# Kernel tuning notes

Hardware: AMD Instinct MI355X
Metric: run time of the kernel (lower is better)

Reference implementation:

```python
import jax, jax.numpy as jnp
import numpy as np

N = 50000
E = 800000
D_IN = 128
D_HID = 128
N_CLASSES = 40


def setup_inputs() -> dict:
    key = jax.random.key(0)
    ks = jax.random.split(key, 8)
    features = jax.random.normal(ks[0], (N, D_IN), dtype=jnp.float32)
    src = jax.random.randint(ks[1], (E,), 0, N)
    dst = jax.random.randint(ks[2], (E,), 0, N)
    edge_index = jnp.stack([src, dst]).astype(jnp.int64)
    def glorot(k, fan_in, fan_out):
        return jax.random.normal(k, (fan_in, fan_out), dtype=jnp.float32) * (1.0 / np.sqrt(fan_in))
    W1 = glorot(ks[3], D_IN, D_HID)
    W2 = glorot(ks[4], D_HID, D_HID)
    W3 = glorot(ks[5], D_HID, N_CLASSES)
    return {
        "features": features,
        "edge_index": edge_index,
        "W1": W1, "b1": jnp.zeros((D_HID,), jnp.float32),
        "W2": W2, "b2": jnp.zeros((D_HID,), jnp.float32),
        "W3": W3, "b3": jnp.zeros((N_CLASSES,), jnp.float32),
    }


def reference(features, edge_index, W1, b1, W2, b2, W3, b3):
    # DGL GraphConv with norm='both': h = D_out^{-1/2} A^T D_in^{-1/2} ... i.e.
    # out[v] = deg_in(v)^{-1/2} * sum_{(u->v) in E} deg_out(u)^{-1/2} * x[u], then @ W + b
    src, dst = edge_index[0], edge_index[1]
    n = features.shape[0]
    ones = jnp.ones((src.shape[0],), features.dtype)
    deg_out = jnp.maximum(jax.ops.segment_sum(ones, src, num_segments=n), 1.0)
    deg_in = jnp.maximum(jax.ops.segment_sum(ones, dst, num_segments=n), 1.0)
    norm_src = deg_out ** -0.5  # [N]
    norm_dst = deg_in ** -0.5   # [N]

    def conv(x, W, b):
        msg = (x * norm_src[:, None])[src]                      # [E, d] gather
        agg = jax.ops.segment_sum(msg, dst, num_segments=n)     # [N, d] scatter-add
        return (agg * norm_dst[:, None]) @ W + b

    # bns=False default -> BatchNorm skipped; dropout p=0.0 -> identity
    h = jax.nn.relu(conv(features, W1, b1))
    h = jax.nn.relu(conv(h, W2, b2))
    return conv(h, W3, b3)  # [N, n_classes]
```

## Files before the change

kernel.cpp:

```cpp
#include <hip/hip_runtime.h>


#define EPB 4096
#define SCAN_CHUNK 4096

typedef short v8s __attribute__((ext_vector_type(8)));
typedef float v4f __attribute__((ext_vector_type(4)));

__device__ __forceinline__ ushort f2bf(float f) {
    unsigned u = __float_as_uint(f);
    unsigned r = (u + 0x7fffu + ((u >> 16) & 1u)) >> 16;
    return (ushort)r;
}
__device__ __forceinline__ void unpack2(unsigned w, float& lo, float& hi) {
    lo = __uint_as_float(w << 16);
    hi = __uint_as_float(w & 0xffff0000u);
}

__global__ __launch_bounds__(256) void front_kernel(const int* __restrict__ ei, int E,
        int nblk1, int NB, int* __restrict__ hist_all,
        ushort* __restrict__ rankD, ushort* __restrict__ rankS,
        const float* __restrict__ W1, const float* __restrict__ W2,
        const float* __restrict__ W3,
        ushort* __restrict__ W1f, ushort* __restrict__ W2f, ushort* __restrict__ W3f) {
    __shared__ int hd[512];
    __shared__ int hs[512];
    int t = threadIdx.x;
    if ((int)blockIdx.x >= nblk1) {
        int idx = ((int)blockIdx.x - nblk1) * 256 + t;
        const float* W; ushort* Wf; int Dout, NF, base;
        if (idx < 2048)      { W = W1; Wf = W1f; Dout = 128; NF = 8; base = idx; }
        else if (idx < 4096) { W = W2; Wf = W2f; Dout = 128; NF = 8; base = idx - 2048; }
        else if (idx < 5120) { W = W3; Wf = W3f; Dout = 40;  NF = 4; base = idx - 4096; }
        else return;
        int lane = base & 63;
        int f = (base >> 6) % NF;
        int ks = base / (64 * NF);
        int c = f * 16 + (lane & 15);
        int kbase = ks * 32 + (lane >> 4) * 8;
        unsigned p[4];
        #pragma unroll
        for (int j = 0; j < 4; ++j) {
            float wlo = (c < Dout) ? W[(size_t)(kbase + 2 * j) * Dout + c] : 0.f;
            float whi = (c < Dout) ? W[(size_t)(kbase + 2 * j + 1) * Dout + c] : 0.f;
            p[j] = (unsigned)f2bf(wlo) | ((unsigned)f2bf(whi) << 16);
        }
        *reinterpret_cast<uint4*>(Wf + (size_t)base * 8) = make_uint4(p[0], p[1], p[2], p[3]);
        return;
    }
    int blk = blockIdx.x;
    for (int i = t; i < 512; i += 256) { hd[i] = 0; hs[i] = 0; }
    __syncthreads();
    int base = blk * EPB;
    #pragma unroll
    for (int j = 0; j < 16; ++j) {
        int e = base + j * 256 + t;
        if (e < E) {
            int s = ei[e], d = ei[E + e];
            rankS[e] = (ushort)atomicAdd(&hs[s >> 8], 1);
            rankD[e] = (ushort)atomicAdd(&hd[d >> 8], 1);
        }
    }
    __syncthreads();
    int L = NB * nblk1;
    for (int b = t; b < NB; b += 256) {
        hist_all[b * nblk1 + blk]     = hd[b];
        hist_all[L + b * nblk1 + blk] = hs[b];
    }
}

__global__ __launch_bounds__(256) void scanA_kernel(const int* __restrict__ data, int L2,
                                                    int* __restrict__ partials) {
    __shared__ int red[256];
    int t = threadIdx.x;
    int base = blockIdx.x * SCAN_CHUNK;
    int s = 0;
    for (int i = t; i < SCAN_CHUNK; i += 256) {
        int idx = base + i;
        if (idx < L2) s += data[idx];
    }
    red[t] = s;
    __syncthreads();
    for (int off = 128; off > 0; off >>= 1) {
        if (t < off) red[t] += red[t + off];
        __syncthreads();
    }
    if (t == 0) partials[blockIdx.x] = red[0];
}

__global__ __launch_bounds__(256) void scanB_kernel(int* __restrict__ partials, int nparts) {
    __shared__ int s[256];
    int t = threadIdx.x;
    s[t] = (t < nparts) ? partials[t] : 0;
    __syncthreads();
    for (int off = 1; off < 256; off <<= 1) {
        int v = (t >= off) ? s[t - off] : 0;
        __syncthreads();
        s[t] += v;
        __syncthreads();
    }
    if (t < nparts) partials[t] = s[t] - partials[t];
}

__global__ __launch_bounds__(256) void scanC_kernel(int* __restrict__ data, int L2,
                                                    const int* __restrict__ partials) {
    __shared__ int tsum[256];
    int t = threadIdx.x;
    int base = blockIdx.x * SCAN_CHUNK + t * 16;
    int local[16];
    int s = 0;
    #pragma unroll
    for (int i = 0; i < 16; ++i) {
        int idx = base + i;
        int v = (idx < L2) ? data[idx] : 0;
        local[i] = v;
        s += v;
    }
    tsum[t] = s;
    __syncthreads();
    for (int off = 1; off < 256; off <<= 1) {
        int v = (t >= off) ? tsum[t - off] : 0;
        __syncthreads();
        tsum[t] += v;
        __syncthreads();
    }
    int run = partials[blockIdx.x] + (t ? tsum[t - 1] : 0);
    #pragma unroll
    for (int i = 0; i < 16; ++i) {
        int idx = base + i;
        if (idx < L2) {
            data[idx] = run;
            run += local[i];
        }
    }
}

template<int NF, int DO_NS, int FP32IN>
__device__ __forceinline__ void mm_body(const void* __restrict__ Xv,
        const ushort* __restrict__ Wf, const float* __restrict__ ns,
        ushort* __restrict__ out, int n, int blk, int wv, int lane) {
    int row0 = (blk * 4 + wv) * 16;
    if (row0 >= n) return;
    int arow = row0 + (lane & 15);
    if (arow >= n) arow = n - 1;
    int kgrp = lane >> 4;
    const v8s* bp = reinterpret_cast<const v8s*>(Wf);
    v4f acc[NF];
    #pragma unroll
    for (int f = 0; f < NF; ++f) acc[f] = (v4f){0.f, 0.f, 0.f, 0.f};
    #pragma unroll
    for (int ks = 0; ks < 4; ++ks) {
        v8s a;
        if (FP32IN) {
            const float* xp = (const float*)Xv + (size_t)arow * 128 + (ks * 4 + kgrp) * 8;
            float4 lo = *reinterpret_cast<const float4*>(xp);
            float4 hi = *reinterpret_cast<const float4*>(xp + 4);
            a[0] = (short)f2bf(lo.x); a[1] = (short)f2bf(lo.y);
            a[2] = (short)f2bf(lo.z); a[3] = (short)f2bf(lo.w);
            a[4] = (short)f2bf(hi.x); a[5] = (short)f2bf(hi.y);
            a[6] = (short)f2bf(hi.z); a[7] = (short)f2bf(hi.w);
        } else {
            const v8s* ap = reinterpret_cast<const v8s*>((const ushort*)Xv + (size_t)arow * 128);
            a = ap[ks * 4 + kgrp];
        }
        #pragma unroll
        for (int f = 0; f < NF; ++f) {
            v8s b = bp[(ks * NF + f) * 64 + lane];
            acc[f] = __builtin_amdgcn_mfma_f32_16x16x32_bf16(a, b, acc[f], 0, 0, 0);
        }
    }
    int rbase = row0 + (lane >> 4) * 4;
    int ccol = lane & 15;
    constexpr int OS = NF * 16;
    #pragma unroll
    for (int r = 0; r < 4; ++r) {
        int gr = rbase + r;
        if (gr < n) {
            float s = DO_NS ? ns[gr] : 1.f;
            #pragma unroll
            for (int f = 0; f < NF; ++f)
                out[(size_t)gr * OS + f * 16 + ccol] = f2bf(s * acc[f][r]);
        }
    }
}

__global__ __launch_bounds__(256) void scatter_mm1_kernel(const int* __restrict__ ei, int E,
        int nblk1, int NB, const int* __restrict__ hist_all,
        const ushort* __restrict__ rankD, const ushort* __restrict__ rankS,
        unsigned* __restrict__ packD, unsigned char* __restrict__ srcb,
        const float* __restrict__ features, const ushort* __restrict__ W1f,
        ushort* __restrict__ xb, int n) {
    int t = threadIdx.x;
    if ((int)blockIdx.x >= nblk1) {
        int blk = (int)blockIdx.x - nblk1;
        mm_body<8, 0, 1>(features, W1f, nullptr, xb, n, blk, t >> 6, t & 63);
        return;
    }
    int blk = blockIdx.x;
    int base = blk * EPB;
    int L = NB * nblk1;
    #pragma unroll
    for (int j = 0; j < 16; ++j) {
        int e = base + j * 256 + t;
        if (e < E) {
            int s = ei[e], d = ei[E + e];
            int posD = hist_all[(d >> 8) * nblk1 + blk] + (int)rankD[e];
            packD[posD] = ((unsigned)(d & 255) << 24) | (unsigned)s;
            int posS = hist_all[L + (s >> 8) * nblk1 + blk] - E + (int)rankS[e];
            srcb[posS] = (unsigned char)(s & 255);
        }
    }
}

__global__ __launch_bounds__(256) void bucket_kernel(const unsigned* __restrict__ packD,
        const unsigned char* __restrict__ srcb, const int* __restrict__ hist_all,
        int nblk1, int NB, int n, int E,
        int* __restrict__ row_ptr, int* __restrict__ col,
        float* __restrict__ norm_src, float* __restrict__ norm_dst) {
    int t = threadIdx.x;
    __shared__ int cnt[256];
    __shared__ int incl[256];
    __shared__ int cur[256];
    if ((int)blockIdx.x < NB) {
        int B = blockIdx.x;
        int s0 = hist_all[B * nblk1];
        int s1 = (B + 1 < NB) ? hist_all[(B + 1) * nblk1] : E;
        cnt[t] = 0;
        __syncthreads();
        for (int i = s0 + t; i < s1; i += 256)
            atomicAdd(&cnt[packD[i] >> 24], 1);
        __syncthreads();
        int v = cnt[t];
        incl[t] = v;
        __syncthreads();
        for (int off = 1; off < 256; off <<= 1) {
            int w = (t >= off) ? incl[t - off] : 0;
            __syncthreads();
            incl[t] += w;
            __syncthreads();
        }
        int excl = incl[t] - v;
        cur[t] = excl;
        int node = B * 256 + t;
        if (node < n) {
            row_ptr[node] = s0 + excl;
            norm_dst[node] = rsqrtf((float)(v > 0 ? v : 1));
        }
        if (B == NB - 1 && t == 0) row_ptr[n] = E;
        __syncthreads();
        for (int i = s0 + t; i < s1; i += 256) {
            unsigned p = packD[i];
            int r = atomicAdd(&cur[p >> 24], 1);
            col[s0 + r] = (int)(p & 0xFFFFFFu);
        }
    } else {
        int B = (int)blockIdx.x - NB;
        int L = NB * nblk1;
        int s0 = hist_all[L + B * nblk1] - E;
        int s1 = (B + 1 < NB) ? (hist_all[L + (B + 1) * nblk1] - E) : E;
        cnt[t] = 0;
        __syncthreads();
        for (int i = s0 + t; i < s1; i += 256)
            atomicAdd(&cnt[srcb[i]], 1);
        __syncthreads();
        int node = B * 256 + t;
        if (node < n) {
            int v = cnt[t];
            norm_src[node] = rsqrtf((float)(v > 0 ? v : 1));
        }
    }
}

template<int EDGE_NS, int ACT_NS, int NF_TOT, int MM_NS, int PAD40>
__global__ __launch_bounds__(256) void aggmm_kernel(const ushort* __restrict__ xt,
        const int* __restrict__ row_ptr, const int* __restrict__ col,
        const float* __restrict__ bias, const float* __restrict__ norm_dst,
        const float* __restrict__ norm_src, const ushort* __restrict__ Wf,
        ushort* __restrict__ out, int n) {
    __shared__ ushort Xl[16][136];
    int t = threadIdx.x;
    int wv = t >> 6, lane = t & 63;
    int row0 = (int)blockIdx.x * 16;
    int quarter = lane >> 4, l4 = lane & 15;
    for (int i = 0; i < 4; ++i) {
        int vi = row0 + wv * 4 + i;
        int lrow = wv * 4 + i;
        if (vi < n) {
            int start = row_ptr[vi], end = row_ptr[vi + 1];
            float acc[8];
            #pragma unroll
            for (int q = 0; q < 8; ++q) acc[q] = 0.f;
            for (int b = start; b < end; b += 64) {
                int m = end - b; if (m > 64) m = 64;
                int u = 0; float s = 1.f;
                if (lane < m) {
                    u = col[b + lane];
                    if (EDGE_NS) s = norm_src[u];
                }
                for (int j = 0; j < m; j += 4) {
                    int jj = j + quarter;
                    int uu = __shfl(u, jj);
                    float ss = EDGE_NS ? __shfl(s, jj) : 1.f;
                    if (jj < m) {
                        const uint4 v = *reinterpret_cast<const uint4*>(xt + (size_t)uu * 128 + 8 * l4);
                        float f0, f1;
                        if (EDGE_NS) {
                            unpack2(v.x, f0, f1); acc[0] = fmaf(ss, f0, acc[0]); acc[1] = fmaf(ss, f1, acc[1]);
                            unpack2(v.y, f0, f1); acc[2] = fmaf(ss, f0, acc[2]); acc[3] = fmaf(ss, f1, acc[3]);
                            unpack2(v.z, f0, f1); acc[4] = fmaf(ss, f0, acc[4]); acc[5] = fmaf(ss, f1, acc[5]);
                            unpack2(v.w, f0, f1); acc[6] = fmaf(ss, f0, acc[6]); acc[7] = fmaf(ss, f1, acc[7]);
                        } else {
                            unpack2(v.x, f0, f1); acc[0] += f0; acc[1] += f1;
                            unpack2(v.y, f0, f1); acc[2] += f0; acc[3] += f1;
                            unpack2(v.z, f0, f1); acc[4] += f0; acc[5] += f1;
                            unpack2(v.w, f0, f1); acc[6] += f0; acc[7] += f1;
                        }
                    }
                }
            }
            #pragma unroll
            for (int q = 0; q < 8; ++q) {
                acc[q] += __shfl_xor(acc[q], 16);
                acc[q] += __shfl_xor(acc[q], 32);
            }
            if (lane < 16) {
                float nd = norm_dst[vi];
                float sc = ACT_NS ? norm_src[vi] : 1.f;
                const float* bp = bias + 8 * lane;
                unsigned p[4];
                #pragma unroll
                for (int q = 0; q < 4; ++q) {
                    float lo = fmaxf(fmaf(nd, acc[2 * q],     bp[2 * q]),     0.f) * sc;
                    float hi = fmaxf(fmaf(nd, acc[2 * q + 1], bp[2 * q + 1]), 0.f) * sc;
                    p[q] = (unsigned)f2bf(lo) | ((unsigned)f2bf(hi) << 16);
                }
                *reinterpret_cast<uint4*>(&Xl[lrow][8 * lane]) = make_uint4(p[0], p[1], p[2], p[3]);
            }
        } else if (lane < 16) {
            *reinterpret_cast<uint4*>(&Xl[lrow][8 * lane]) = make_uint4(0, 0, 0, 0);
        }
    }
    __syncthreads();
    constexpr int FPW = NF_TOT / 4;
    const v8s* bp = reinterpret_cast<const v8s*>(Wf);
    int kgrp = lane >> 4;
    v4f acc[FPW];
    #pragma unroll
    for (int f = 0; f < FPW; ++f) acc[f] = (v4f){0.f, 0.f, 0.f, 0.f};
    #pragma unroll
    for (int ks = 0; ks < 4; ++ks) {
        v8s a = *reinterpret_cast<const v8s*>(&Xl[lane & 15][(ks * 4 + kgrp) * 8]);
        #pragma unroll
        for (int f = 0; f < FPW; ++f) {
            int F = wv * FPW + f;
            v8s b = bp[(ks * NF_TOT + F) * 64 + lane];
            acc[f] = __builtin_amdgcn_mfma_f32_16x16x32_bf16(a, b, acc[f], 0, 0, 0);
        }
    }
    int rbase = row0 + (lane >> 4) * 4;
    int ccol = lane & 15;
    constexpr int OS = NF_TOT * 16;
    #pragma unroll
    for (int r = 0; r < 4; ++r) {
        int gr = rbase + r;
        if (gr < n) {
            float s = MM_NS ? norm_src[gr] : 1.f;
            #pragma unroll
            for (int f = 0; f < FPW; ++f) {
                int colo = (wv * FPW + f) * 16 + ccol;
                ushort val = f2bf(s * acc[f][r]);
                if (PAD40 && colo >= 40) val = 0;
                out[(size_t)gr * OS + colo] = val;
            }
        }
    }
}

__global__ __launch_bounds__(256) void agg40_kernel(const ushort* __restrict__ yb,
        const int* __restrict__ row_ptr, const int* __restrict__ col,
        const float* __restrict__ norm_dst, const float* __restrict__ b3,
        float* __restrict__ out, int n) {
    int wid  = (blockIdx.x * blockDim.x + threadIdx.x) >> 6;
    int lane = threadIdx.x & 63;
    if (wid >= n) return;
    int start = row_ptr[wid], end = row_ptr[wid + 1];
    int oct = lane >> 3, l8 = lane & 7;
    float acc[8];
    #pragma unroll
    for (int i = 0; i < 8; ++i) acc[i] = 0.f;
    for (int b = start; b < end; b += 64) {
        int m = end - b; if (m > 64) m = 64;
        int u = 0;
        if (lane < m) u = col[b + lane];
        for (int j = 0; j < m; j += 8) {
            int jj = j + oct;
            int uu = __shfl(u, jj);
            if (jj < m) {
                const uint4 v = *reinterpret_cast<const uint4*>(yb + (size_t)uu * 64 + 8 * l8);
                float f0, f1;
                unpack2(v.x, f0, f1); acc[0] += f0; acc[1] += f1;
                unpack2(v.y, f0, f1); acc[2] += f0; acc[3] += f1;
                unpack2(v.z, f0, f1); acc[4] += f0; acc[5] += f1;
                unpack2(v.w, f0, f1); acc[6] += f0; acc[7] += f1;
            }
        }
    }
    #pragma unroll
    for (int i = 0; i < 8; ++i) {
        acc[i] += __shfl_xor(acc[i], 8);
        acc[i] += __shfl_xor(acc[i], 16);
        acc[i] += __shfl_xor(acc[i], 32);
    }
    if (lane < 5) {
        float nd = norm_dst[wid];
        const float* bp = b3 + 8 * lane;
        float* op = out + (size_t)wid * 40 + 8 * lane;
        float4 o0, o1;
        o0.x = fmaf(nd, acc[0], bp[0]); o0.y = fmaf(nd, acc[1], bp[1]);
        o0.z = fmaf(nd, acc[2], bp[2]); o0.w = fmaf(nd, acc[3], bp[3]);
        o1.x = fmaf(nd, acc[4], bp[4]); o1.y = fmaf(nd, acc[5], bp[5]);
        o1.z = fmaf(nd, acc[6], bp[6]); o1.w = fmaf(nd, acc[7], bp[7]);
        *reinterpret_cast<float4*>(op)     = o0;
        *reinterpret_cast<float4*>(op + 4) = o1;
    }
}

extern "C" void kernel_launch(void* const* d_in, const int* in_sizes, int n_in,
                              void* d_out, int out_size, void* d_ws, size_t ws_size,
                              hipStream_t stream) {
    const float* features = (const float*)d_in[0];
    const int*   ei       = (const int*)d_in[1];
    const float* W1 = (const float*)d_in[2];
    const float* b1 = (const float*)d_in[3];
    const float* W2 = (const float*)d_in[4];
    const float* b2 = (const float*)d_in[5];
    const float* W3 = (const float*)d_in[6];
    const float* b3 = (const float*)d_in[7];

    const int n = in_sizes[0] / 128;
    const int E = in_sizes[1] / 2;

    const int nblk1 = (E + EPB - 1) / EPB;
    const int NB    = (n + 255) >> 8;
    const int L     = NB * nblk1;
    const int L2    = 2 * L;
    const int sb2   = (L2 + SCAN_CHUNK - 1) / SCAN_CHUNK;

    char* w = (char*)d_ws;
    auto alloc = [&](size_t bytes) {
        char* p = w;
        w += (bytes + 255) & ~(size_t)255;
        return p;
    };
    int*    hist_all = (int*)   alloc((size_t)L2 * 4);
    int*    partials = (int*)   alloc((size_t)256 * 4);
    float*  norm_src = (float*) alloc((size_t)n * 4);
    float*  norm_dst = (float*) alloc((size_t)n * 4);
    int*    row_ptr  = (int*)   alloc((size_t)(n + 1) * 4);
    int*    col      = (int*)   alloc((size_t)E * 4);
    ushort* xb1      = (ushort*)alloc((size_t)n * 128 * 2);
    ushort* xb2      = (ushort*)alloc((size_t)n * 128 * 2);
    char*   scratch  = (char*)  alloc((size_t)12 * E);
    ushort* W1f      = (ushort*)alloc((size_t)16384 * 2);
    ushort* W2f      = (ushort*)alloc((size_t)16384 * 2);
    ushort* W3f      = (ushort*)alloc((size_t)8192 * 2);

    char* scr = scratch;
    ushort*        rankD = (ushort*)scr;                 scr += ((size_t)E * 2 + 255) & ~(size_t)255;
    ushort*        rankS = (ushort*)scr;                 scr += ((size_t)E * 2 + 255) & ~(size_t)255;
    unsigned*      packD = (unsigned*)scr;               scr += ((size_t)E * 4 + 255) & ~(size_t)255;
    unsigned char* srcb  = (unsigned char*)scr;
    ushort* yb = (ushort*)scratch;

    int mmb = (n + 63) / 64;
    int fb  = (n + 15) / 16;
    int ab  = (n + 3) / 4;

    front_kernel<<<nblk1 + 20, 256, 0, stream>>>(ei, E, nblk1, NB, hist_all,
                                                 rankD, rankS, W1, W2, W3, W1f, W2f, W3f);
    scanA_kernel<<<sb2, 256, 0, stream>>>(hist_all, L2, partials);
    scanB_kernel<<<1, 256, 0, stream>>>(partials, sb2);
    scanC_kernel<<<sb2, 256, 0, stream>>>(hist_all, L2, partials);
    scatter_mm1_kernel<<<nblk1 + mmb, 256, 0, stream>>>(ei, E, nblk1, NB, hist_all,
                                                        rankD, rankS, packD, srcb,
                                                        features, W1f, xb1, n);
    bucket_kernel<<<2 * NB, 256, 0, stream>>>(packD, srcb, hist_all, nblk1, NB, n, E,
                                              row_ptr, col, norm_src, norm_dst);
    aggmm_kernel<1, 0, 8, 1, 0><<<fb, 256, 0, stream>>>(xb1, row_ptr, col, b1,
                                                        norm_dst, norm_src, W2f, xb2, n);
    aggmm_kernel<0, 1, 4, 0, 1><<<fb, 256, 0, stream>>>(xb2, row_ptr, col, b2,
                                                        norm_dst, norm_src, W3f, yb, n);
    agg40_kernel<<<ab, 256, 0, stream>>>(yb, row_ptr, col, norm_dst, b3, (float*)d_out, n);
}
```

Baseline: 164.1 us.

## Give each wave its own 16-row tile in fused aggregate-matmul kernel

The aggregate+MFMA kernel now assigns each wavefront an independent 16-node tile with its own LDS buffer, so the block-wide barrier between the gather and matmul phases is removed. Each wave then computes all output column fragments itself, and the block count drops to cover 64 nodes per block. The gather is also reshaped so 8 lanes cover one neighbor row with two 16-byte loads each, handling 8 neighbors per step instead of 4. In exchange, every wave loads the full weight matrix and holds more accumulator registers, which may lower occupancy.

```diff
diff --git a/kernel.cpp b/kernel.cpp
--- a/kernel.cpp
+++ b/kernel.cpp
@@ -271,25 +271,25 @@
     }
 }
 
-template<int EDGE_NS, int ACT_NS, int NF_TOT, int MM_NS, int PAD40>
+template<int EDGE_NS, int ACT_NS, int NF, int MM_NS, int PAD40>
 __global__ __launch_bounds__(256) void aggmm_kernel(const ushort* __restrict__ xt,
         const int* __restrict__ row_ptr, const int* __restrict__ col,
         const float* __restrict__ bias, const float* __restrict__ norm_dst,
         const float* __restrict__ norm_src, const ushort* __restrict__ Wf,
         ushort* __restrict__ out, int n) {
-    __shared__ ushort Xl[16][136];
+    __shared__ ushort Xl[4][16][136];
     int t = threadIdx.x;
     int wv = t >> 6, lane = t & 63;
-    int row0 = (int)blockIdx.x * 16;
-    int quarter = lane >> 4, l4 = lane & 15;
-    for (int i = 0; i < 4; ++i) {
-        int vi = row0 + wv * 4 + i;
-        int lrow = wv * 4 + i;
+    int vbase = ((int)blockIdx.x * 4 + wv) * 16;
+    if (vbase >= n) return;
+    int oct = lane >> 3, l8 = lane & 7;
+    for (int i = 0; i < 16; ++i) {
+        int vi = vbase + i;
         if (vi < n) {
             int start = row_ptr[vi], end = row_ptr[vi + 1];
-            float acc[8];
+            float acc[16];
             #pragma unroll
-            for (int q = 0; q < 8; ++q) acc[q] = 0.f;
+            for (int q = 0; q < 16; ++q) acc[q] = 0.f;
             for (int b = start; b < end; b += 64) {
                 int m = end - b; if (m > 64) m = 64;
                 int u = 0; float s = 1.f;
@@ -297,78 +297,90 @@
                     u = col[b + lane];
                     if (EDGE_NS) s = norm_src[u];
                 }
-                for (int j = 0; j < m; j += 4) {
-                    int jj = j + quarter;
+                for (int j = 0; j < m; j += 8) {
+                    int jj = j + oct;
                     int uu = __shfl(u, jj);
                     float ss = EDGE_NS ? __shfl(s, jj) : 1.f;
                     if (jj < m) {
-                        const uint4 v = *reinterpret_cast<const uint4*>(xt + (size_t)uu * 128 + 8 * l4);
+                        const ushort* rp = xt + (size_t)uu * 128 + 16 * l8;
+                        uint4 v0 = *reinterpret_cast<const uint4*>(rp);
+                        uint4 v1 = *reinterpret_cast<const uint4*>(rp + 8);
                         float f0, f1;
                         if (EDGE_NS) {
-                            unpack2(v.x, f0, f1); acc[0] = fmaf(ss, f0, acc[0]); acc[1] = fmaf(ss, f1, acc[1]);
-                            unpack2(v.y, f0, f1); acc[2] = fmaf(ss, f0, acc[2]); acc[3] = fmaf(ss, f1, acc[3]);
-                            unpack2(v.z, f0, f1); acc[4] = fmaf(ss, f0, acc[4]); acc[5] = fmaf(ss, f1, acc[5]);
-                            unpack2(v.w, f0, f1); acc[6] = fmaf(ss, f0, acc[6]); acc[7] = fmaf(ss, f1, acc[7]);
+                            unpack2(v0.x, f0, f1); acc[0]  = fmaf(ss, f0, acc[0]);  acc[1]  = fmaf(ss, f1, acc[1]);
+                            unpack2(v0.y, f0, f1); acc[2]  = fmaf(ss, f0, acc[2]);  acc[3]  = fmaf(ss, f1, acc[3]);
+                            unpack2(v0.z, f0, f1); acc[4]  = fmaf(ss, f0, acc[4]);  acc[5]  = fmaf(ss, f1, acc[5]);
+                            unpack2(v0.w, f0, f1); acc[6]  = fmaf(ss, f0, acc[6]);  acc[7]  = fmaf(ss, f1, acc[7]);
+                            unpack2(v1.x, f0, f1); acc[8]  = fmaf(ss, f0, acc[8]);  acc[9]  = fmaf(ss, f1, acc[9]);
+                            unpack2(v1.y, f0, f1); acc[10] = fmaf(ss, f0, acc[10]); acc[11] = fmaf(ss, f1, acc[11]);
+                            unpack2(v1.z, f0, f1); acc[12] = fmaf(ss, f0, acc[12]); acc[13] = fmaf(ss, f1, acc[13]);
+                            unpack2(v1.w, f0, f1); acc[14] = fmaf(ss, f0, acc[14]); acc[15] = fmaf(ss, f1, acc[15]);
                         } else {
-                            unpack2(v.x, f0, f1); acc[0] += f0; acc[1] += f1;
-                            unpack2(v.y, f0, f1); acc[2] += f0; acc[3] += f1;
-                            unpack2(v.z, f0, f1); acc[4] += f0; acc[5] += f1;
-                            unpack2(v.w, f0, f1); acc[6] += f0; acc[7] += f1;
+                            unpack2(v0.x, f0, f1); acc[0]  += f0; acc[1]  += f1;
+                            unpack2(v0.y, f0, f1); acc[2]  += f0; acc[3]  += f1;
+                            unpack2(v0.z, f0, f1); acc[4]  += f0; acc[5]  += f1;
+                            unpack2(v0.w, f0, f1); acc[6]  += f0; acc[7]  += f1;
+                            unpack2(v1.x, f0, f1); acc[8]  += f0; acc[9]  += f1;
+                            unpack2(v1.y, f0, f1); acc[10] += f0; acc[11] += f1;
+                            unpack2(v1.z, f0, f1); acc[12] += f0; acc[13] += f1;
+                            unpack2(v1.w, f0, f1); acc[14] += f0; acc[15] += f1;
                         }
                     }
                 }
             }
             #pragma unroll
-            for (int q = 0; q < 8; ++q) {
+            for (int q = 0; q < 16; ++q) {
+                acc[q] += __shfl_xor(acc[q], 8);
                 acc[q] += __shfl_xor(acc[q], 16);
                 acc[q] += __shfl_xor(acc[q], 32);
             }
-            if (lane < 16) {
+            if (oct == 0) {
                 float nd = norm_dst[vi];
                 float sc = ACT_NS ? norm_src[vi] : 1.f;
-                const float* bp = bias + 8 * lane;
-                unsigned p[4];
+                const float* bp = bias + 16 * l8;
+                unsigned p[8];
                 #pragma unroll
-                for (int q = 0; q < 4; ++q) {
+                for (int q = 0; q < 8; ++q) {
                     float lo = fmaxf(fmaf(nd, acc[2 * q],     bp[2 * q]),     0.f) * sc;
                     float hi = fmaxf(fmaf(nd, acc[2 * q + 1], bp[2 * q + 1]), 0.f) * sc;
                     p[q] = (unsigned)f2bf(lo) | ((unsigned)f2bf(hi) << 16);
                 }
-                *reinterpret_cast<uint4*>(&Xl[lrow][8 * lane]) = make_uint4(p[0], p[1], p[2], p[3]);
+                uint4* lp = reinterpret_cast<uint4*>(&Xl[wv][i][16 * l8]);
+                lp[0] = make_uint4(p[0], p[1], p[2], p[3]);
+                lp[1] = make_uint4(p[4], p[5], p[6], p[7]);
             }
-        } else if (lane < 16) {
-            *reinterpret_cast<uint4*>(&Xl[lrow][8 * lane]) = make_uint4(0, 0, 0, 0);
-        }
-    }
-    __syncthreads();
-    constexpr int FPW = NF_TOT / 4;
-    const v8s* bp = reinterpret_cast<const v8s*>(Wf);
+        } else if (oct == 0) {
+            uint4* lp = reinterpret_cast<uint4*>(&Xl[wv][i][16 * l8]);
+            lp[0] = make_uint4(0, 0, 0, 0);
+            lp[1] = make_uint4(0, 0, 0, 0);
+        }
+    }
+    const v8s* bp2 = reinterpret_cast<const v8s*>(Wf);
     int kgrp = lane >> 4;
-    v4f acc[FPW];
-    #pragma unroll
-    for (int f = 0; f < FPW; ++f) acc[f] = (v4f){0.f, 0.f, 0.f, 0.f};
+    v4f macc[NF];
+    #pragma unroll
+    for (int f = 0; f < NF; ++f) macc[f] = (v4f){0.f, 0.f, 0.f, 0.f};
     #pragma unroll
     for (int ks = 0; ks < 4; ++ks) {
-        v8s a = *reinterpret_cast<const v8s*>(&Xl[lane & 15][(ks * 4 + kgrp) * 8]);
+        v8s a = *reinterpret_cast<const v8s*>(&Xl[wv][lane & 15][(ks * 4 + kgrp) * 8]);
         #pragma unroll
-        for (int f = 0; f < FPW; ++f) {
-            int F = wv * FPW + f;
-            v8s b = bp[(ks * NF_TOT + F) * 64 + lane];
-            acc[f] = __builtin_amdgcn_mfma_f32_16x16x32_bf16(a, b, acc[f], 0, 0, 0);
-        }
-    }
-    int rbase = row0 + (lane >> 4) * 4;
+        for (int f = 0; f < NF; ++f) {
+            v8s b = bp2[(ks * NF + f) * 64 + lane];
+            macc[f] = __builtin_amdgcn_mfma_f32_16x16x32_bf16(a, b, macc[f], 0, 0, 0);
+        }
+    }
+    int rbase = vbase + (lane >> 4) * 4;
     int ccol = lane & 15;
-    constexpr int OS = NF_TOT * 16;
+    constexpr int OS = NF * 16;
     #pragma unroll
     for (int r = 0; r < 4; ++r) {
         int gr = rbase + r;
         if (gr < n) {
             float s = MM_NS ? norm_src[gr] : 1.f;
             #pragma unroll
-            for (int f = 0; f < FPW; ++f) {
-                int colo = (wv * FPW + f) * 16 + ccol;
-                ushort val = f2bf(s * acc[f][r]);
+            for (int f = 0; f < NF; ++f) {
+                int colo = f * 16 + ccol;
+                ushort val = f2bf(s * macc[f][r]);
                 if (PAD40 && colo >= 40) val = 0;
                 out[(size_t)gr * OS + colo] = val;
             }
@@ -473,7 +485,7 @@
     ushort* yb = (ushort*)scratch;
 
     int mmb = (n + 63) / 64;
-    int fb  = (n + 15) / 16;
+    int fb  = (n + 63) / 64;
     int ab  = (n + 3) / 4;
 
     front_kernel<<<nblk1 + 20, 256, 0, stream>>>(ei, E, nblk1, NB, hist_all,
```

Measured after the change: 210.0 us. 28.0% more time.

## Assign one node per lane group in aggregation and fold scan offsets into scanC

Applied to the files above, without the earlier changes.

The aggregation in both aggmm_kernel and agg40_kernel now gives each node its own 16-lane (or 8-lane) group, which walks that node's edges two at a time with dual accumulators. This replaces the old scheme where a whole wave shared one node and reduced partial sums with cross-lane shuffles. The change removes those shuffle reductions and the serial per-node loop, and puts more independent node work in flight per wave. The trade-off is divergence when degrees vary across the nodes in a wave. Separately, the scanB launch is removed: thread 0 of each scanC block now sums the preceding partials serially, saving one kernel launch at the cost of a short serial loop per block.

```diff
diff --git a/kernel.cpp b/kernel.cpp
--- a/kernel.cpp
+++ b/kernel.cpp
@@ -88,24 +88,16 @@
     if (t == 0) partials[blockIdx.x] = red[0];
 }
 
-__global__ __launch_bounds__(256) void scanB_kernel(int* __restrict__ partials, int nparts) {
-    __shared__ int s[256];
-    int t = threadIdx.x;
-    s[t] = (t < nparts) ? partials[t] : 0;
-    __syncthreads();
-    for (int off = 1; off < 256; off <<= 1) {
-        int v = (t >= off) ? s[t - off] : 0;
-        __syncthreads();
-        s[t] += v;
-        __syncthreads();
-    }
-    if (t < nparts) partials[t] = s[t] - partials[t];
-}
-
 __global__ __launch_bounds__(256) void scanC_kernel(int* __restrict__ data, int L2,
                                                     const int* __restrict__ partials) {
     __shared__ int tsum[256];
-    int t = threadIdx.x;
+    __shared__ int baseoff;
+    int t = threadIdx.x;
+    if (t == 0) {
+        int s = 0;
+        for (int i = 0; i < (int)blockIdx.x; ++i) s += partials[i];
+        baseoff = s;
+    }
     int base = blockIdx.x * SCAN_CHUNK + t * 16;
     int local[16];
     int s = 0;
@@ -124,7 +116,7 @@
         tsum[t] += v;
         __syncthreads();
     }
-    int run = partials[blockIdx.x] + (t ? tsum[t - 1] : 0);
+    int run = baseoff + (t ? tsum[t - 1] : 0);
     #pragma unroll
     for (int i = 0; i < 16; ++i) {
         int idx = base + i;
@@ -282,67 +274,75 @@
     int wv = t >> 6, lane = t & 63;
     int row0 = (int)blockIdx.x * 16;
     int quarter = lane >> 4, l4 = lane & 15;
-    for (int i = 0; i < 4; ++i) {
-        int vi = row0 + wv * 4 + i;
-        int lrow = wv * 4 + i;
-        if (vi < n) {
-            int start = row_ptr[vi], end = row_ptr[vi + 1];
-            float acc[8];
-            #pragma unroll
-            for (int q = 0; q < 8; ++q) acc[q] = 0.f;
-            for (int b = start; b < end; b += 64) {
-                int m = end - b; if (m > 64) m = 64;
-                int u = 0; float s = 1.f;
-                if (lane < m) {
-                    u = col[b + lane];
-                    if (EDGE_NS) s = norm_src[u];
-                }
-                for (int j = 0; j < m; j += 4) {
-                    int jj = j + quarter;
-                    int uu = __shfl(u, jj);
-                    float ss = EDGE_NS ? __shfl(s, jj) : 1.f;
-                    if (jj < m) {
-                        const uint4 v = *reinterpret_cast<const uint4*>(xt + (size_t)uu * 128 + 8 * l4);
-                        float f0, f1;
-                        if (EDGE_NS) {
-                            unpack2(v.x, f0, f1); acc[0] = fmaf(ss, f0, acc[0]); acc[1] = fmaf(ss, f1, acc[1]);
-                            unpack2(v.y, f0, f1); acc[2] = fmaf(ss, f0, acc[2]); acc[3] = fmaf(ss, f1, acc[3]);
-                            unpack2(v.z, f0, f1); acc[4] = fmaf(ss, f0, acc[4]); acc[5] = fmaf(ss, f1, acc[5]);
-                            unpack2(v.w, f0, f1); acc[6] = fmaf(ss, f0, acc[6]); acc[7] = fmaf(ss, f1, acc[7]);
-                        } else {
-                            unpack2(v.x, f0, f1); acc[0] += f0; acc[1] += f1;
-                            unpack2(v.y, f0, f1); acc[2] += f0; acc[3] += f1;
-                            unpack2(v.z, f0, f1); acc[4] += f0; acc[5] += f1;
-                            unpack2(v.w, f0, f1); acc[6] += f0; acc[7] += f1;
-                        }
-                    }
-                }
+    int vi = row0 + wv * 4 + quarter;
+    int lrow = wv * 4 + quarter;
+    if (vi < n) {
+        int start = row_ptr[vi], end = row_ptr[vi + 1];
+        float a0[8], a1[8];
+        #pragma unroll
+        for (int q = 0; q < 8; ++q) { a0[q] = 0.f; a1[q] = 0.f; }
+        int e = start;
+        for (; e + 2 <= end; e += 2) {
+            int u0 = col[e], u1 = col[e + 1];
+            float s0 = EDGE_NS ? norm_src[u0] : 1.f;
+            float s1 = EDGE_NS ? norm_src[u1] : 1.f;
+            const uint4 v0 = *reinterpret_cast<const uint4*>(xt + (size_t)u0 * 128 + 8 * l4);
+            const uint4 v1 = *reinterpret_cast<const uint4*>(xt + (size_t)u1 * 128 + 8 * l4);
+            float f0, f1;
+            if (EDGE_NS) {
+                unpack2(v0.x, f0, f1); a0[0] = fmaf(s0, f0, a0[0]); a0[1] = fmaf(s0, f1, a0[1]);
+                unpack2(v0.y, f0, f1); a0[2] = fmaf(s0, f0, a0[2]); a0[3] = fmaf(s0, f1, a0[3]);
+                unpack2(v0.z, f0, f1); a0[4] = fmaf(s0, f0, a0[4]); a0[5] = fmaf(s0, f1, a0[5]);
+                unpack2(v0.w, f0, f1); a0[6] = fmaf(s0, f0, a0[6]); a0[7] = fmaf(s0, f1, a0[7]);
+                unpack2(v1.x, f0, f1); a1[0] = fmaf(s1, f0, a1[0]); a1[1] = fmaf(s1, f1, a1[1]);
+                unpack2(v1.y, f0, f1); a1[2] = fmaf(s1, f0, a1[2]); a1[3] = fmaf(s1, f1, a1[3]);
+                unpack2(v1.z, f0, f1); a1[4] = fmaf(s1, f0, a1[4]); a1[5] = fmaf(s1, f1, a1[5]);
+                unpack2(v1.w, f0, f1); a1[6] = fmaf(s1, f0, a1[6]); a1[7] = fmaf(s1, f1, a1[7]);
+            } else {
+                unpack2(v0.x, f0, f1); a0[0] += f0; a0[1] += f1;
+                unpack2(v0.y, f0, f1); a0[2] += f0; a0[3] += f1;
+                unpack2(v0.z, f0, f1); a0[4] += f0; a0[5] += f1;
+                unpack2(v0.w, f0, f1); a0[6] += f0; a0[7] += f1;
+                unpack2(v1.x, f0, f1); a1[0] += f0; a1[1] += f1;
+                unpack2(v1.y, f0, f1); a1[2] += f0; a1[3] += f1;
+                unpack2(v1.z, f0, f1); a1[4] += f0; a1[5] += f1;
+                unpack2(v1.w, f0, f1); a1[6] += f0; a1[7] += f1;
             }
-            #pragma unroll
-            for (int q = 0; q < 8; ++q) {
-                acc[q] += __shfl_xor(acc[q], 16);
-                acc[q] += __shfl_xor(acc[q], 32);
+        }
+        if (e < end) {
+            int u0 = col[e];
+            float s0 = EDGE_NS ? norm_src[u0] : 1.f;
+            const uint4 v0 = *reinterpret_cast<const uint4*>(xt + (size_t)u0 * 128 + 8 * l4);
+            float f0, f1;
+            if (EDGE_NS) {
+                unpack2(v0.x, f0, f1); a0[0] = fmaf(s0, f0, a0[0]); a0[1] = fmaf(s0, f1, a0[1]);
+                unpack2(v0.y, f0, f1); a0[2] = fmaf(s0, f0, a0[2]); a0[3] = fmaf(s0, f1, a0[3]);
+                unpack2(v0.z, f0, f1); a0[4] = fmaf(s0, f0, a0[4]); a0[5] = fmaf(s0, f1, a0[5]);
+                unpack2(v0.w, f0, f1); a0[6] = fmaf(s0, f0, a0[6]); a0[7] = fmaf(s0, f1, a0[7]);
+            } else {
+                unpack2(v0.x, f0, f1); a0[0] += f0; a0[1] += f1;
+                unpack2(v0.y, f0, f1); a0[2] += f0; a0[3] += f1;
+                unpack2(v0.z, f0, f1); a0[4] += f0; a0[5] += f1;
+                unpack2(v0.w, f0, f1); a0[6] += f0; a0[7] += f1;
             }
-            if (lane < 16) {
-                float nd = norm_dst[vi];
-                float sc = ACT_NS ? norm_src[vi] : 1.f;
-                const float* bp = bias + 8 * lane;
-                unsigned p[4];
-                #pragma unroll
-                for (int q = 0; q < 4; ++q) {
-                    float lo = fmaxf(fmaf(nd, acc[2 * q],     bp[2 * q]),     0.f) * sc;
-                    float hi = fmaxf(fmaf(nd, acc[2 * q + 1], bp[2 * q + 1]), 0.f) * sc;
-                    p[q] = (unsigned)f2bf(lo) | ((unsigned)f2bf(hi) << 16);
-                }
-                *reinterpret_cast<uint4*>(&Xl[lrow][8 * lane]) = make_uint4(p[0], p[1], p[2], p[3]);
-            }
-        } else if (lane < 16) {
-            *reinterpret_cast<uint4*>(&Xl[lrow][8 * lane]) = make_uint4(0, 0, 0, 0);
-        }
+        }
+        float nd = norm_dst[vi];
+        float sc = ACT_NS ? norm_src[vi] : 1.f;
+        const float* bp = bias + 8 * l4;
+        unsigned p[4];
+        #pragma unroll
+        for (int q = 0; q < 4; ++q) {
+            float lo = fmaxf(fmaf(nd, a0[2 * q]     + a1[2 * q],     bp[2 * q]),     0.f) * sc;
+            float hi = fmaxf(fmaf(nd, a0[2 * q + 1] + a1[2 * q + 1], bp[2 * q + 1]), 0.f) * sc;
+            p[q] = (unsigned)f2bf(lo) | ((unsigned)f2bf(hi) << 16);
+        }
+        *reinterpret_cast<uint4*>(&Xl[lrow][16 * l4 / 2]) = make_uint4(p[0], p[1], p[2], p[3]);
+    } else {
+        *reinterpret_cast<uint4*>(&Xl[lrow][8 * l4]) = make_uint4(0, 0, 0, 0);
     }
     __syncthreads();
     constexpr int FPW = NF_TOT / 4;
-    const v8s* bp = reinterpret_cast<const v8s*>(Wf);
+    const v8s* bp2 = reinterpret_cast<const v8s*>(Wf);
     int kgrp = lane >> 4;
     v4f acc[FPW];
     #pragma unroll
@@ -353,7 +353,7 @@
         #pragma unroll
         for (int f = 0; f < FPW; ++f) {
             int F = wv * FPW + f;
-            v8s b = bp[(ks * NF_TOT + F) * 64 + lane];
+            v8s b = bp2[(ks * NF_TOT + F) * 64 + lane];
             acc[f] = __builtin_amdgcn_mfma_f32_16x16x32_bf16(a, b, acc[f], 0, 0, 0);
         }
     }
@@ -380,46 +380,48 @@
         const int* __restrict__ row_ptr, const int* __restrict__ col,
         const float* __restrict__ norm_dst, const float* __restrict__ b3,
         float* __restrict__ out, int n) {
-    int wid  = (blockIdx.x * blockDim.x + threadIdx.x) >> 6;
-    int lane = threadIdx.x & 63;
-    if (wid >= n) return;
-    int start = row_ptr[wid], end = row_ptr[wid + 1];
+    int t = threadIdx.x;
+    int wv = t >> 6, lane = t & 63;
     int oct = lane >> 3, l8 = lane & 7;
-    float acc[8];
-    #pragma unroll
-    for (int i = 0; i < 8; ++i) acc[i] = 0.f;
-    for (int b = start; b < end; b += 64) {
-        int m = end - b; if (m > 64) m = 64;
-        int u = 0;
-        if (lane < m) u = col[b + lane];
-        for (int j = 0; j < m; j += 8) {
-            int jj = j + oct;
-            int uu = __shfl(u, jj);
-            if (jj < m) {
-                const uint4 v = *reinterpret_cast<const uint4*>(yb + (size_t)uu * 64 + 8 * l8);
-                float f0, f1;
-                unpack2(v.x, f0, f1); acc[0] += f0; acc[1] += f1;
-                unpack2(v.y, f0, f1); acc[2] += f0; acc[3] += f1;
-                unpack2(v.z, f0, f1); acc[4] += f0; acc[5] += f1;
-                unpack2(v.w, f0, f1); acc[6] += f0; acc[7] += f1;
-            }
-        }
-    }
-    #pragma unroll
-    for (int i = 0; i < 8; ++i) {
-        acc[i] += __shfl_xor(acc[i], 8);
-        acc[i] += __shfl_xor(acc[i], 16);
-        acc[i] += __shfl_xor(acc[i], 32);
-    }
-    if (lane < 5) {
-        float nd = norm_dst[wid];
-        const float* bp = b3 + 8 * lane;
-        float* op = out + (size_t)wid * 40 + 8 * lane;
+    int vi = (int)blockIdx.x * 32 + wv * 8 + oct;
+    if (vi >= n) return;
+    int start = row_ptr[vi], end = row_ptr[vi + 1];
+    float a0[8], a1[8];
+    #pragma unroll
+    for (int i = 0; i < 8; ++i) { a0[i] = 0.f; a1[i] = 0.f; }
+    int e = start;
+    for (; e + 2 <= end; e += 2) {
+        int u0 = col[e], u1 = col[e + 1];
+        const uint4 v0 = *reinterpret_cast<const uint4*>(yb + (size_t)u0 * 64 + 8 * l8);
+        const uint4 v1 = *reinterpret_cast<const uint4*>(yb + (size_t)u1 * 64 + 8 * l8);
+        float f0, f1;
+        unpack2(v0.x, f0, f1); a0[0] += f0; a0[1] += f1;
+        unpack2(v0.y, f0, f1); a0[2] += f0; a0[3] += f1;
+        unpack2(v0.z, f0, f1); a0[4] += f0; a0[5] += f1;
+        unpack2(v0.w, f0, f1); a0[6] += f0; a0[7] += f1;
+        unpack2(v1.x, f0, f1); a1[0] += f0; a1[1] += f1;
+        unpack2(v1.y, f0, f1); a1[2] += f0; a1[3] += f1;
+        unpack2(v1.z, f0, f1); a1[4] += f0; a1[5] += f1;
+        unpack2(v1.w, f0, f1); a1[6] += f0; a1[7] += f1;
+    }
+    if (e < end) {
+        int u0 = col[e];
+        const uint4 v0 = *reinterpret_cast<const uint4*>(yb + (size_t)u0 * 64 + 8 * l8);
+        float f0, f1;
+        unpack2(v0.x, f0, f1); a0[0] += f0; a0[1] += f1;
+        unpack2(v0.y, f0, f1); a0[2] += f0; a0[3] += f1;
+        unpack2(v0.z, f0, f1); a0[4] += f0; a0[5] += f1;
+        unpack2(v0.w, f0, f1); a0[6] += f0; a0[7] += f1;
+    }
+    if (l8 < 5) {
+        float nd = norm_dst[vi];
+        const float* bp = b3 + 8 * l8;
+        float* op = out + (size_t)vi * 40 + 8 * l8;
         float4 o0, o1;
-        o0.x = fmaf(nd, acc[0], bp[0]); o0.y = fmaf(nd, acc[1], bp[1]);
-        o0.z = fmaf(nd, acc[2], bp[2]); o0.w = fmaf(nd, acc[3], bp[3]);
-        o1.x = fmaf(nd, acc[4], bp[4]); o1.y = fmaf(nd, acc[5], bp[5]);
-        o1.z = fmaf(nd, acc[6], bp[6]); o1.w = fmaf(nd, acc[7], bp[7]);
+        o0.x = fmaf(nd, a0[0] + a1[0], bp[0]); o0.y = fmaf(nd, a0[1] + a1[1], bp[1]);
+        o0.z = fmaf(nd, a0[2] + a1[2], bp[2]); o0.w = fmaf(nd, a0[3] + a1[3], bp[3]);
+        o1.x = fmaf(nd, a0[4] + a1[4], bp[4]); o1.y = fmaf(nd, a0[5] + a1[5], bp[5]);
+        o1.z = fmaf(nd, a0[6] + a1[6], bp[6]); o1.w = fmaf(nd, a0[7] + a1[7], bp[7]);
         *reinterpret_cast<float4*>(op)     = o0;
         *reinterpret_cast<float4*>(op + 4) = o1;
     }
@@ -472,14 +474,13 @@
     unsigned char* srcb  = (unsigned char*)scr;
     ushort* yb = (ushort*)scratch;
 
-    int mmb = (n + 63) / 64;
-    int fb  = (n + 15) / 16;
-    int ab  = (n + 3) / 4;
+    int mmb  = (n + 63) / 64;
+    int fb   = (n + 15) / 16;
+    int ab40 = (n + 31) / 32;
 
     front_kernel<<<nblk1 + 20, 256, 0, stream>>>(ei, E, nblk1, NB, hist_all,
                                                  rankD, rankS, W1, W2, W3, W1f, W2f, W3f);
     scanA_kernel<<<sb2, 256, 0, stream>>>(hist_all, L2, partials);
-    scanB_kernel<<<1, 256, 0, stream>>>(partials, sb2);
     scanC_kernel<<<sb2, 256, 0, stream>>>(hist_all, L2, partials);
     scatter_mm1_kernel<<<nblk1 + mmb, 256, 0, stream>>>(ei, E, nblk1, NB, hist_all,
                                                         rankD, rankS, packD, srcb,
@@ -490,5 +491,5 @@
                                                         norm_dst, norm_src, W2f, xb2, n);
     aggmm_kernel<0, 1, 4, 0, 1><<<fb, 256, 0, stream>>>(xb2, row_ptr, col, b2,
                                                         norm_dst, norm_src, W3f, yb, n);
-    agg40_kernel<<<ab, 256, 0, stream>>>(yb, row_ptr, col, norm_dst, b3, (float*)d_out, n);
-}
+    agg40_kernel<<<ab40, 256, 0, stream>>>(yb, row_ptr, col, norm_dst, b3, (float*)d_out, n);
+}
```

Result: faster. 148.9 us (-9.3%).
